# Kernel optimization log

Measured on AMD Instinct MI355X. Metric: run time of the kernel, lower is better.

## Reference

```python
import jax, jax.numpy as jnp
import numpy as np

EPS32 = np.float32(np.finfo(np.float32).eps)
N, D_IN = 8192, 256
LAYERS = [256, 128, 64]


def setup_inputs() -> dict:
    key = jax.random.key(0)
    ks = jax.random.split(key, 16)
    inp = {
        "feat_matrix": jax.random.normal(ks[0], (N, D_IN), dtype=jnp.float32),
        "adj_matrix": jnp.zeros((1,), jnp.float32),
        "get_item_index": jnp.zeros((1,), jnp.int64),
        "set_index": jnp.zeros((1,), jnp.int64),
        "val_index": jnp.zeros((1,), jnp.int64),
        "mask_matrix": jnp.zeros((1,), jnp.float32),
    }
    # Linear params for each (gl, gnn) pair, kaiming-ish scale 1/sqrt(fan_in)
    ki = 1
    for li in range(len(LAYERS) - 1):
        fi, fo = LAYERS[li], LAYERS[li + 1]
        s = 1.0 / np.sqrt(fi)
        inp[f"Wgl{li}"] = jax.random.uniform(ks[ki], (fi, fo), jnp.float32, -s, s); ki += 1
        inp[f"bgl{li}"] = jax.random.uniform(ks[ki], (fo,), jnp.float32, -s, s); ki += 1
        inp[f"Wgnn{li}"] = jax.random.uniform(ks[ki], (fi, fo), jnp.float32, -s, s); ki += 1
        inp[f"bgnn{li}"] = jax.random.uniform(ks[ki], (fo,), jnp.float32, -s, s); ki += 1
    inp["temp"] = jnp.float32(0.1)
    inp["theta"] = jnp.float32(0.1)
    return inp


def _cdgm_forward(x, params, temp, theta):
    n_layers = len(params)
    for k, (Wgl, bgl, Wgnn, bgnn) in enumerate(params):
        gl = jax.nn.relu(x @ Wgl + bgl)                      # [N, F]
        # pairwise squared distances without materializing [N, N, F]
        sq = jnp.sum(gl * gl, axis=-1)                       # [N]
        diff = jnp.maximum(sq[:, None] + sq[None, :] - 2.0 * (gl @ gl.T), 0.0)  # [N, N]
        mask = (diff != 0.0).astype(diff.dtype)
        dist = -jnp.sqrt(diff + EPS32) * mask
        adj = jax.nn.sigmoid((1.0 + temp) * dist + (5.0 + theta))  # [N, N]
        deg = jnp.sum(adj, axis=-1)                          # [N]; diag-inverse == rowwise divide
        x = (adj @ (x @ Wgnn + bgnn)) / deg[:, None]
        if k != n_layers - 1:
            x = jax.nn.relu(x)
    return jax.nn.softmax(x, axis=-1)


def reference(feat_matrix, adj_matrix, get_item_index, set_index, val_index, mask_matrix,
              Wgl0, bgl0, Wgnn0, bgnn0, Wgl1, bgl1, Wgnn1, bgnn1, temp, theta):
    params = [(Wgl0, bgl0, Wgnn0, bgnn0), (Wgl1, bgl1, Wgnn1, bgnn1)]
    return _cdgm_forward(feat_matrix, params, temp, theta)
```

## Files before the change

### kernel.cpp

```cpp
#include <hip/hip_runtime.h>
#include <hip/hip_bf16.h>

#define NROWS 8192

typedef __bf16 bf16x8 __attribute__((ext_vector_type(8)));
typedef float f32x4 __attribute__((ext_vector_type(4)));
typedef unsigned short ushort_t;
typedef unsigned int uint_t;

__device__ __forceinline__ ushort_t f2bf(float f) {
  uint_t u = __builtin_bit_cast(uint_t, f);
  u += 0x7fffu + ((u >> 16) & 1u);
  return (ushort_t)(u >> 16);
}
__device__ __forceinline__ float bf2f(ushort_t h) {
  uint_t u = ((uint_t)h) << 16;
  return __builtin_bit_cast(float, u);
}
__device__ __forceinline__ void load_lds16(const ushort_t* g, ushort_t* l) {
  __builtin_amdgcn_global_load_lds(
      (const __attribute__((address_space(1))) unsigned int*)g,
      (__attribute__((address_space(3))) unsigned int*)l, 16, 0, 0);
}
__device__ __forceinline__ void load_lds4(const float* g, float* l) {
  __builtin_amdgcn_global_load_lds(
      (const __attribute__((address_space(1))) unsigned int*)g,
      (__attribute__((address_space(3))) unsigned int*)l, 4, 0, 0);
}

template<int DIN, int F>
__global__ __launch_bounds__(256) void prep_w_kernel(
    const float* __restrict__ W1, const float* __restrict__ W2,
    ushort_t* __restrict__ Wf)
{
  constexpr int NCT = (2 * F) / 16;
  int idx = blockIdx.x * 256 + threadIdx.x;
  int e = idx & 7, lane = (idx >> 3) & 63;
  int ct = (idx >> 9) % NCT, kk = (idx >> 9) / NCT;
  int g = lane >> 4, q = lane & 15;
  int k = 32 * kk + 8 * g + e, c = 16 * ct + q;
  float v = (c < F) ? W1[(size_t)k * F + c] : W2[(size_t)k * F + (c - F)];
  Wf[idx] = f2bf(v);
}

template<int DIN, int F, bool RED>
__global__ __launch_bounds__(256) void lin_kernel(
    const float* __restrict__ x, const ushort_t* __restrict__ Wf,
    const float* __restrict__ b1, const float* __restrict__ b2,
    ushort_t* __restrict__ glf, float* __restrict__ sq, ushort_t* __restrict__ hf)
{
  constexpr int Fp   = F + 16;
  constexpr int NT   = Fp / 16;
  constexpr int KK   = F / 32;
  constexpr int KKD  = DIN / 32;
  constexpr int NCT  = (2 * F) / 16;
  constexpr int NCTW = NCT / 4;
  __shared__ float    xs[16][DIN];
  __shared__ float    hs[16][F];
  __shared__ ushort_t gls[16][F];
  __shared__ float    sqs[16];
  __shared__ float    degs[16];
  const int t  = threadIdx.x;
  const int m  = blockIdx.x;
  const int r0 = m * 16;
  const int w = t >> 6, lane = t & 63, g = lane >> 4, q = lane & 15;

  if (RED) {
    constexpr size_t STR = (size_t)NROWS * 144;
    if (t < 16) {
      float d = 0.f;
#pragma unroll
      for (int js = 0; js < 8; ++js)
        d += x[js * STR + (size_t)(r0 + t) * 144 + 128];
      degs[t] = d;
    }
    __syncthreads();
    for (int i = t; i < 16 * DIN; i += 256) {
      int r = i / DIN, c = i % DIN;
      float s = 0.f;
#pragma unroll
      for (int js = 0; js < 8; ++js)
        s += x[js * STR + (size_t)(r0 + r) * 144 + c];
      xs[r][c] = fmaxf(s, 0.f) / degs[r];
    }
  } else {
    for (int i = t; i < 16 * DIN; i += 256)
      xs[i / DIN][i % DIN] = x[(size_t)(r0 + i / DIN) * DIN + (i % DIN)];
  }
  if (t < 16) sqs[t] = 0.f;
  __syncthreads();

  bf16x8 aF[KKD];
#pragma unroll
  for (int kk = 0; kk < KKD; ++kk) {
    const float* src = &xs[q][32 * kk + 8 * g];
    __align__(16) ushort_t tmp[8];
#pragma unroll
    for (int e = 0; e < 8; ++e) tmp[e] = f2bf(src[e]);
    aF[kk] = *(const bf16x8*)tmp;
  }
  f32x4 acc[NCTW];
#pragma unroll
  for (int tl = 0; tl < NCTW; ++tl) {
    int c = 16 * (NCTW * w + tl) + q;
    float bv = (c < F) ? b1[c] : b2[c - F];
    acc[tl] = (f32x4){bv, bv, bv, bv};
  }
#pragma unroll
  for (int kk = 0; kk < KKD; ++kk)
#pragma unroll
    for (int tl = 0; tl < NCTW; ++tl) {
      bf16x8 bW = *(const bf16x8*)(Wf +
          ((size_t)(kk * NCT) + (NCTW * w + tl)) * 512 + lane * 8);
      acc[tl] = __builtin_amdgcn_mfma_f32_16x16x32_bf16(aF[kk], bW, acc[tl], 0, 0, 0);
    }
#pragma unroll
  for (int tl = 0; tl < NCTW; ++tl)
#pragma unroll
    for (int r = 0; r < 4; ++r) {
      int row = 4 * g + r, c = 16 * (NCTW * w + tl) + q;
      float v = acc[tl][r];
      if (c < F) {
        float gv = fmaxf(v, 0.f);
        ushort_t gb = f2bf(gv);
        gls[row][c] = gb;
        float gf = bf2f(gb);
        atomicAdd(&sqs[row], gf * gf);
      } else {
        hs[row][c - F] = v;
      }
    }
  __syncthreads();
  if (t < 16) sq[r0 + t] = sqs[t];

  {
    constexpr int CH = KK * 64;
    if (t < CH) {
      int kk = t >> 6, li = t & 63;
      int row = li & 15, c0 = 32 * kk + 8 * (li >> 4);
      uint4 v = *(const uint4*)&gls[row][c0];
      *(uint4*)(glf + ((size_t)(m * KK + kk) * 64 + li) * 8) = v;
    }
  }
  {
    const int jc  = m >> 2;
    const int P   = (m >> 1) & 1;
    const int glo = (m & 1) * 2;
    for (int idx = t; idx < NT * 32; idx += 256) {
      int t2 = idx >> 5, li = idx & 31;
      int gg = li >> 4, qq = li & 15;
      int feat = 16 * t2 + qq;
      ushort_t tmp[8];
#pragma unroll
      for (int e = 0; e < 8; ++e) {
        if (feat < F)        tmp[e] = f2bf(hs[8 * gg + e][feat]);
        else if (feat == F)  tmp[e] = (ushort_t)0x3F80;
        else                 tmp[e] = 0;
      }
      int ln = (glo + gg) * 16 + qq;
      uint4* dst = (uint4*)(hf + ((size_t)((jc * 2 + P) * NT + t2) * 64 + ln) * 8);
      *dst = *(const uint4*)tmp;
    }
  }
}

template<int F>
__global__ __launch_bounds__(256) void fused_kernel(
    const ushort_t* __restrict__ glf, const float* __restrict__ sq,
    const ushort_t* __restrict__ hf,
    const float* __restrict__ temp_p, const float* __restrict__ theta_p,
    float* __restrict__ partial)
{
  constexpr int Fp   = F + 16;
  constexpr int NT   = Fp / 16;
  constexpr int KK   = F / 32;
  constexpr int JS   = 8;
  constexpr int JCH  = NROWS / JS;
  constexpr int NIT  = JCH / 32;
  constexpr int NCHB = 2 * KK;
  constexpr int NHF  = NT - 1;
  constexpr int NCH  = NCHB + NHF;
  constexpr float EPS = 1.1920929e-07f;
  constexpr float LOG2E = 1.4426950408889634f;
  __shared__ __align__(16) ushort_t stage[NCH * 512 + 128];
  __shared__ __align__(16) ushort_t adjlds[128 * 32];

  const int w = threadIdx.x >> 6, lane = threadIdx.x & 63;
  const int g = lane >> 4, q = lane & 15;
  const int n  = blockIdx.x + (int)gridDim.x * blockIdx.y;
  const int bx = n >> 3, by = n & 7;
  const int irow  = bx * 128 + 32 * w;
  const int jbase = by * JCH;
  const float c1 = 1.0f + *temp_p;
  const float c0 = 5.0f + *theta_p;
  const float k1 = c1 * LOG2E;
  const float k0 = -c0 * LOG2E;

  bf16x8 aF[2][KK];
#pragma unroll
  for (int s = 0; s < 2; ++s)
#pragma unroll
    for (int kk = 0; kk < KK; ++kk)
      aF[s][kk] = *(const bf16x8*)(glf +
          ((size_t)(((irow >> 4) + s) * KK + kk) * 64 + lane) * 8);
  float sqi[2][4];
#pragma unroll
  for (int s = 0; s < 2; ++s)
#pragma unroll
    for (int r = 0; r < 4; ++r) sqi[s][r] = sq[irow + 16 * s + 4 * g + r] + EPS;

  bf16x8 onesF;
  {
    __align__(16) ushort_t tmp[8];
    ushort_t v = (q == 0) ? (ushort_t)0x3F80 : (ushort_t)0;
#pragma unroll
    for (int e = 0; e < 8; ++e) tmp[e] = v;
    onesF = *(const bf16x8*)tmp;
  }

  ushort_t* wp[8];
#pragma unroll
  for (int tt = 0; tt < 2; ++tt)
#pragma unroll
    for (int r = 0; r < 4; ++r) {
      int row = 32 * w + 4 * g + r;
      int colb = 32 * tt + 2 * q;
      wp[tt * 4 + r] = (ushort_t*)((char*)adjlds
                        + row * 64 + (colb ^ (((row >> 2) & 3) << 4)));
    }
  const ushort_t* rp;
  {
    int row = 32 * w + q;
    rp = (const ushort_t*)((char*)adjlds
          + row * 64 + ((16 * g) ^ (((row >> 2) & 3) << 4)));
  }
  const float* sql = (const float*)(stage + NCH * 512) + q;

  f32x4 acc[2][NT];
#pragma unroll
  for (int s = 0; s < 2; ++s)
#pragma unroll
    for (int i = 0; i < NT; ++i) acc[s][i] = (f32x4){0.f, 0.f, 0.f, 0.f};

#pragma unroll 1
  for (int k = 0; k < NIT; ++k) {
    const int j0 = jbase + k * 32;
    __syncthreads();
    {
      const ushort_t* glB = glf + (size_t)(j0 >> 4) * KK * 512;
      const ushort_t* glH = hf  + (size_t)(j0 >> 5) * NT * 512;
#pragma unroll
      for (int ch = w; ch < NCH; ch += 4) {
        const ushort_t* src = (ch < NCHB) ? (glB + (size_t)ch * 512)
                                          : (glH + (size_t)(ch - NCHB) * 512);
        load_lds16(src + lane * 8, stage + ch * 512);
      }
      if (w == 3 && lane < 32)
        load_lds4(sq + j0 + lane, (float*)(stage + NCH * 512) + lane);
    }
    __syncthreads();

    f32x4 sA[2][2];
    float sqj[2];
#pragma unroll
    for (int tt = 0; tt < 2; ++tt) {
      sqj[tt] = sql[16 * tt];
      f32x4 c0a = (f32x4){0.f, 0.f, 0.f, 0.f};
      f32x4 c1a = (f32x4){0.f, 0.f, 0.f, 0.f};
#pragma unroll
      for (int kk = 0; kk < KK; ++kk) {
        bf16x8 b = *(const bf16x8*)(stage + (tt * KK + kk) * 512 + lane * 8);
        c0a = __builtin_amdgcn_mfma_f32_16x16x32_bf16(aF[0][kk], b, c0a, 0, 0, 0);
        c1a = __builtin_amdgcn_mfma_f32_16x16x32_bf16(aF[1][kk], b, c1a, 0, 0, 0);
      }
      sA[0][tt] = c0a;
      sA[1][tt] = c1a;
    }
#pragma unroll
    for (int s = 0; s < 2; ++s)
#pragma unroll
      for (int tt = 0; tt < 2; ++tt)
#pragma unroll
        for (int r = 0; r < 4; ++r) {
          float t1 = sqi[s][r] + sqj[tt];
          float d  = fmaxf(fmaf(-2.f, sA[s][tt][r], t1), EPS);
          float e  = __builtin_amdgcn_exp2f(
                       fmaf(k1, __builtin_amdgcn_sqrtf(d), k0));
          float adjv = __builtin_amdgcn_rcpf(1.f + e);
          uint_t u = __builtin_bit_cast(uint_t, adjv) + 0x8000u;
          *(wp[tt * 4 + r] + s * 512) = (ushort_t)(u >> 16);
        }
    asm volatile("s_waitcnt lgkmcnt(0)" ::: "memory");
    {
      bf16x8 aP0 = *(const bf16x8*)(rp);
      bf16x8 aP1 = *(const bf16x8*)(rp + 512);
#pragma unroll
      for (int t2 = 0; t2 < NT; ++t2) {
        bf16x8 hF = (t2 == NT - 1)
            ? onesF
            : *(const bf16x8*)(stage + (NCHB + t2) * 512 + lane * 8);
        acc[0][t2] = __builtin_amdgcn_mfma_f32_16x16x32_bf16(aP0, hF, acc[0][t2], 0, 0, 0);
        acc[1][t2] = __builtin_amdgcn_mfma_f32_16x16x32_bf16(aP1, hF, acc[1][t2], 0, 0, 0);
      }
    }
  }

  float* op = partial + ((size_t)by * NROWS + irow) * Fp;
#pragma unroll
  for (int s = 0; s < 2; ++s)
#pragma unroll
    for (int t2 = 0; t2 < NT; ++t2)
#pragma unroll
      for (int r = 0; r < 4; ++r)
        op[(size_t)(16 * s + 4 * g + r) * Fp + 16 * t2 + q] = acc[s][t2][r];
}

__global__ __launch_bounds__(256) void reduce_softmax_kernel(
    const float* __restrict__ partial, float* __restrict__ out)
{
  int t = threadIdx.x;
  int r = blockIdx.x * 4 + (t >> 6), c = t & 63;
  size_t base = (size_t)r * 80;
  size_t stride = (size_t)NROWS * 80;
  float v = 0.f, d = 0.f;
#pragma unroll
  for (int js = 0; js < 8; ++js) {
    v += partial[js * stride + base + c];
    d += partial[js * stride + base + 64];
  }
  v /= d;
  float m = v;
  for (int o = 32; o > 0; o >>= 1) m = fmaxf(m, __shfl_xor(m, o, 64));
  float e = __expf(v - m);
  float s = e;
  for (int o = 32; o > 0; o >>= 1) s += __shfl_xor(s, o, 64);
  out[(size_t)r * 64 + c] = e / s;
}

extern "C" void kernel_launch(void* const* d_in, const int* in_sizes, int n_in,
                              void* d_out, int out_size, void* d_ws, size_t ws_size,
                              hipStream_t stream) {
  const float* feat  = (const float*)d_in[0];
  const float* Wgl0  = (const float*)d_in[6];
  const float* bgl0  = (const float*)d_in[7];
  const float* Wgnn0 = (const float*)d_in[8];
  const float* bgnn0 = (const float*)d_in[9];
  const float* Wgl1  = (const float*)d_in[10];
  const float* bgl1  = (const float*)d_in[11];
  const float* Wgnn1 = (const float*)d_in[12];
  const float* bgnn1 = (const float*)d_in[13];
  const float* temp  = (const float*)d_in[14];
  const float* theta = (const float*)d_in[15];
  float* out = (float*)d_out;

  char* ws = (char*)d_ws;
  size_t off = 0;
  auto alloc = [&](size_t bytes) {
    char* p = ws + off;
    off = (off + bytes + 255) & ~(size_t)255;
    return p;
  };
  float*    par0 = (float*)alloc(8ull * NROWS * 144 * 4);
  float*    par1 = par0;
  ushort_t* glf0 = (ushort_t*)alloc((8192ull / 16) * 4 * 64 * 8 * 2);
  ushort_t* glf1 = (ushort_t*)alloc((8192ull / 16) * 2 * 64 * 8 * 2);
  ushort_t* hf0  = (ushort_t*)alloc((8192ull / 64) * 2 * 9 * 64 * 8 * 2);
  ushort_t* hf1  = (ushort_t*)alloc((8192ull / 64) * 2 * 5 * 64 * 8 * 2);
  float*    sq0  = (float*)alloc(8192ull * 4);
  float*    sq1  = (float*)alloc(8192ull * 4);
  ushort_t* Wf0  = (ushort_t*)alloc(8ull * 16 * 512 * 2);
  ushort_t* Wf1  = (ushort_t*)alloc(4ull * 8 * 512 * 2);

  prep_w_kernel<256, 128><<<256, 256, 0, stream>>>(Wgl0, Wgnn0, Wf0);
  prep_w_kernel<128, 64><<<64, 256, 0, stream>>>(Wgl1, Wgnn1, Wf1);

  lin_kernel<256, 128, false><<<512, 256, 0, stream>>>(feat, Wf0, bgl0, bgnn0, glf0, sq0, hf0);
  fused_kernel<128><<<dim3(64, 8), 256, 0, stream>>>(glf0, sq0, hf0, temp, theta, par0);

  lin_kernel<128, 64, true><<<512, 256, 0, stream>>>(par0, Wf1, bgl1, bgnn1, glf1, sq1, hf1);
  fused_kernel<64><<<dim3(64, 8), 256, 0, stream>>>(glf1, sq1, hf1, temp, theta, par1);
  reduce_softmax_kernel<<<2048, 256, 0, stream>>>(par1, out);
}
```

Before: 142.6 us.

## Switch fused distance/aggregation kernel to 32x32x16 MFMA with in-register adjacency

The fused kernel now computes the pairwise Gram tile with 32x32x16 bf16 MFMA instead of 16x16x32. It converts the sigmoid adjacency values into the A-operand layout with packed bf16 conversion and permlane32 swaps, so the adjacency tile no longer goes through LDS. Its aim is to drop the LDS write/wait/read round trip and cut the MFMA issue count. The glf/hf staging layouts in lin_kernel and the partial-output stride (now padded to 32-column multiples) change to match, which adds some extra partial traffic and reduction work downstream.

```diff
diff --git a/kernel.cpp b/kernel.cpp
--- a/kernel.cpp
+++ b/kernel.cpp
@@ -5,6 +5,9 @@
 
 typedef __bf16 bf16x8 __attribute__((ext_vector_type(8)));
 typedef float f32x4 __attribute__((ext_vector_type(4)));
+typedef float f32x16 __attribute__((ext_vector_type(16)));
+typedef unsigned int u32x2 __attribute__((ext_vector_type(2)));
+typedef unsigned int u32x4 __attribute__((ext_vector_type(4)));
 typedef unsigned short ushort_t;
 typedef unsigned int uint_t;
 
@@ -16,6 +19,11 @@
 __device__ __forceinline__ float bf2f(ushort_t h) {
   uint_t u = ((uint_t)h) << 16;
   return __builtin_bit_cast(float, u);
+}
+__device__ __forceinline__ uint_t cvtpk(float lo, float hi) {
+  uint_t r;
+  asm("v_cvt_pk_bf16_f32 %0, %1, %2" : "=v"(r) : "v"(lo), "v"(hi));
+  return r;
 }
 __device__ __forceinline__ void load_lds16(const ushort_t* g, ushort_t* l) {
   __builtin_amdgcn_global_load_lds(
@@ -47,14 +55,12 @@
 __global__ __launch_bounds__(256) void lin_kernel(
     const float* __restrict__ x, const ushort_t* __restrict__ Wf,
     const float* __restrict__ b1, const float* __restrict__ b2,
-    ushort_t* __restrict__ glf, float* __restrict__ sq, ushort_t* __restrict__ hf)
+    ushort_t* __restrict__ glf32, float* __restrict__ sq, ushort_t* __restrict__ hf32)
 {
-  constexpr int Fp   = F + 16;
-  constexpr int NT   = Fp / 16;
-  constexpr int KK   = F / 32;
   constexpr int KKD  = DIN / 32;
   constexpr int NCT  = (2 * F) / 16;
   constexpr int NCTW = NCT / 4;
+  constexpr int FT   = F / 32;
   __shared__ float    xs[16][DIN];
   __shared__ float    hs[16][F];
   __shared__ ushort_t gls[16][F];
@@ -66,12 +72,12 @@
   const int w = t >> 6, lane = t & 63, g = lane >> 4, q = lane & 15;
 
   if (RED) {
-    constexpr size_t STR = (size_t)NROWS * 144;
+    constexpr size_t STR = (size_t)NROWS * 160;
     if (t < 16) {
       float d = 0.f;
 #pragma unroll
       for (int js = 0; js < 8; ++js)
-        d += x[js * STR + (size_t)(r0 + t) * 144 + 128];
+        d += x[js * STR + (size_t)(r0 + t) * 160 + 128];
       degs[t] = d;
     }
     __syncthreads();
@@ -80,7 +86,7 @@
       float s = 0.f;
 #pragma unroll
       for (int js = 0; js < 8; ++js)
-        s += x[js * STR + (size_t)(r0 + r) * 144 + c];
+        s += x[js * STR + (size_t)(r0 + r) * 160 + c];
       xs[r][c] = fmaxf(s, 0.f) / degs[r];
     }
   } else {
@@ -133,60 +139,43 @@
   __syncthreads();
   if (t < 16) sq[r0 + t] = sqs[t];
 
-  {
-    constexpr int CH = KK * 64;
-    if (t < CH) {
-      int kk = t >> 6, li = t & 63;
-      int row = li & 15, c0 = 32 * kk + 8 * (li >> 4);
-      uint4 v = *(const uint4*)&gls[row][c0];
-      *(uint4*)(glf + ((size_t)(m * KK + kk) * 64 + li) * 8) = v;
-    }
-  }
-  {
-    const int jc  = m >> 2;
-    const int P   = (m >> 1) & 1;
-    const int glo = (m & 1) * 2;
-    for (int idx = t; idx < NT * 32; idx += 256) {
-      int t2 = idx >> 5, li = idx & 31;
-      int gg = li >> 4, qq = li & 15;
-      int feat = 16 * t2 + qq;
-      ushort_t tmp[8];
-#pragma unroll
-      for (int e = 0; e < 8; ++e) {
-        if (feat < F)        tmp[e] = f2bf(hs[8 * gg + e][feat]);
-        else if (feat == F)  tmp[e] = (ushort_t)0x3F80;
-        else                 tmp[e] = 0;
-      }
-      int ln = (glo + gg) * 16 + qq;
-      uint4* dst = (uint4*)(hf + ((size_t)((jc * 2 + P) * NT + t2) * 64 + ln) * 8);
-      *dst = *(const uint4*)tmp;
-    }
+  if (t < 32 * (F / 16)) {
+    int ch = t >> 5, li = t & 31;
+    int lane2 = 32 * (li >> 4) + 16 * (m & 1) + (li & 15);
+    const uint4* src = (const uint4*)&gls[li & 15][16 * ch + 8 * (li >> 4)];
+    *(uint4*)(glf32 + ((size_t)(m >> 1) * (F / 16) + ch) * 512 + lane2 * 8) = *src;
+  }
+  if (t < FT * 64) {
+    int ft = t >> 6, l2 = t & 63;
+    __align__(16) ushort_t tmp[8];
+#pragma unroll
+    for (int e = 0; e < 8; ++e)
+      tmp[e] = f2bf(hs[8 * (l2 >> 5) + e][32 * ft + (l2 & 31)]);
+    *(uint4*)(hf32 + ((size_t)m * FT + ft) * 512 + l2 * 8) = *(const uint4*)tmp;
   }
 }
 
 template<int F>
 __global__ __launch_bounds__(256) void fused_kernel(
-    const ushort_t* __restrict__ glf, const float* __restrict__ sq,
-    const ushort_t* __restrict__ hf,
+    const ushort_t* __restrict__ glf32, const float* __restrict__ sq,
+    const ushort_t* __restrict__ hf32,
     const float* __restrict__ temp_p, const float* __restrict__ theta_p,
     float* __restrict__ partial)
 {
-  constexpr int Fp   = F + 16;
-  constexpr int NT   = Fp / 16;
-  constexpr int KK   = F / 32;
+  constexpr int FT   = F / 32;
+  constexpr int FpO  = 32 * (FT + 1);
+  constexpr int KKW  = F / 16;
   constexpr int JS   = 8;
   constexpr int JCH  = NROWS / JS;
   constexpr int NIT  = JCH / 32;
-  constexpr int NCHB = 2 * KK;
-  constexpr int NHF  = NT - 1;
-  constexpr int NCH  = NCHB + NHF;
+  constexpr int NCHB = KKW;
+  constexpr int NCH  = NCHB + 2 * FT;
   constexpr float EPS = 1.1920929e-07f;
   constexpr float LOG2E = 1.4426950408889634f;
   __shared__ __align__(16) ushort_t stage[NCH * 512 + 128];
-  __shared__ __align__(16) ushort_t adjlds[128 * 32];
 
   const int w = threadIdx.x >> 6, lane = threadIdx.x & 63;
-  const int g = lane >> 4, q = lane & 15;
+  const int hi = lane >> 5, col = lane & 31;
   const int n  = blockIdx.x + (int)gridDim.x * blockIdx.y;
   const int bx = n >> 3, by = n & 7;
   const int irow  = bx * 128 + 32 * w;
@@ -196,59 +185,37 @@
   const float k1 = c1 * LOG2E;
   const float k0 = -c0 * LOG2E;
 
-  bf16x8 aF[2][KK];
-#pragma unroll
-  for (int s = 0; s < 2; ++s)
-#pragma unroll
-    for (int kk = 0; kk < KK; ++kk)
-      aF[s][kk] = *(const bf16x8*)(glf +
-          ((size_t)(((irow >> 4) + s) * KK + kk) * 64 + lane) * 8);
-  float sqi[2][4];
-#pragma unroll
-  for (int s = 0; s < 2; ++s)
-#pragma unroll
-    for (int r = 0; r < 4; ++r) sqi[s][r] = sq[irow + 16 * s + 4 * g + r] + EPS;
+  bf16x8 iF[KKW];
+#pragma unroll
+  for (int kk = 0; kk < KKW; ++kk)
+    iF[kk] = *(const bf16x8*)(glf32 +
+        ((size_t)(irow >> 5) * KKW + kk) * 512 + lane * 8);
+  const float sqi = sq[irow + col] + EPS;
 
   bf16x8 onesF;
   {
     __align__(16) ushort_t tmp[8];
-    ushort_t v = (q == 0) ? (ushort_t)0x3F80 : (ushort_t)0;
+    ushort_t v = (col == 0) ? (ushort_t)0x3F80 : (ushort_t)0;
 #pragma unroll
     for (int e = 0; e < 8; ++e) tmp[e] = v;
     onesF = *(const bf16x8*)tmp;
   }
 
-  ushort_t* wp[8];
-#pragma unroll
-  for (int tt = 0; tt < 2; ++tt)
-#pragma unroll
-    for (int r = 0; r < 4; ++r) {
-      int row = 32 * w + 4 * g + r;
-      int colb = 32 * tt + 2 * q;
-      wp[tt * 4 + r] = (ushort_t*)((char*)adjlds
-                        + row * 64 + (colb ^ (((row >> 2) & 3) << 4)));
-    }
-  const ushort_t* rp;
-  {
-    int row = 32 * w + q;
-    rp = (const ushort_t*)((char*)adjlds
-          + row * 64 + ((16 * g) ^ (((row >> 2) & 3) << 4)));
-  }
-  const float* sql = (const float*)(stage + NCH * 512) + q;
-
-  f32x4 acc[2][NT];
-#pragma unroll
-  for (int s = 0; s < 2; ++s)
-#pragma unroll
-    for (int i = 0; i < NT; ++i) acc[s][i] = (f32x4){0.f, 0.f, 0.f, 0.f};
+  f32x16 acc[FT + 1];
+#pragma unroll
+  for (int ft = 0; ft <= FT; ++ft)
+#pragma unroll
+    for (int r = 0; r < 16; ++r) acc[ft][r] = 0.f;
+
+  const float* sqlane = (const float*)(stage + NCH * 512) + 4 * hi;
 
 #pragma unroll 1
   for (int k = 0; k < NIT; ++k) {
     const int j0 = jbase + k * 32;
     __syncthreads();
     {
-      const ushort_t* glB = glf + (size_t)(j0 >> 4) * KK * 512;
-      const ushort_t* glH = hf  + (size_t)(j0 >> 5) * NT * 512;
+      const ushort_t* glB = glf32 + (size_t)(j0 >> 5) * KKW * 512;
+      const ushort_t* glH = hf32  + (size_t)(j0 >> 4) * FT * 512;
 #pragma unroll
       for (int ch = w; ch < NCH; ch += 4) {
         const ushort_t* src = (ch < NCHB) ? (glB + (size_t)ch * 512)
@@ -260,59 +227,58 @@
     }
     __syncthreads();
 
-    f32x4 sA[2][2];
-    float sqj[2];
-#pragma unroll
-    for (int tt = 0; tt < 2; ++tt) {
-      sqj[tt] = sql[16 * tt];
-      f32x4 c0a = (f32x4){0.f, 0.f, 0.f, 0.f};
-      f32x4 c1a = (f32x4){0.f, 0.f, 0.f, 0.f};
-#pragma unroll
-      for (int kk = 0; kk < KK; ++kk) {
-        bf16x8 b = *(const bf16x8*)(stage + (tt * KK + kk) * 512 + lane * 8);
-        c0a = __builtin_amdgcn_mfma_f32_16x16x32_bf16(aF[0][kk], b, c0a, 0, 0, 0);
-        c1a = __builtin_amdgcn_mfma_f32_16x16x32_bf16(aF[1][kk], b, c1a, 0, 0, 0);
+    f32x16 sacc;
+#pragma unroll
+    for (int r = 0; r < 16; ++r) sacc[r] = 0.f;
+#pragma unroll
+    for (int kk = 0; kk < KKW; ++kk) {
+      bf16x8 jf = *(const bf16x8*)(stage + kk * 512 + lane * 8);
+      sacc = __builtin_amdgcn_mfma_f32_32x32x16_bf16(jf, iF[kk], sacc, 0, 0, 0);
+    }
+    f32x4 sqjv[4];
+#pragma unroll
+    for (int G = 0; G < 4; ++G) sqjv[G] = *(const f32x4*)(sqlane + 8 * G);
+    float adjv[16];
+#pragma unroll
+    for (int r = 0; r < 16; ++r) {
+      float t1 = sqi + sqjv[r >> 2][r & 3];
+      float d  = fmaxf(fmaf(-2.f, sacc[r], t1), EPS);
+      float e  = __builtin_amdgcn_exp2f(fmaf(k1, __builtin_amdgcn_sqrtf(d), k0));
+      adjv[r] = __builtin_amdgcn_rcpf(1.f + e);
+    }
+    uint_t P0 = cvtpk(adjv[0],  adjv[1]),  P1 = cvtpk(adjv[2],  adjv[3]);
+    uint_t P2 = cvtpk(adjv[4],  adjv[5]),  P3 = cvtpk(adjv[6],  adjv[7]);
+    uint_t P4 = cvtpk(adjv[8],  adjv[9]),  P5 = cvtpk(adjv[10], adjv[11]);
+    uint_t P6 = cvtpk(adjv[12], adjv[13]), P7 = cvtpk(adjv[14], adjv[15]);
+    u32x2 sA0 = __builtin_amdgcn_permlane32_swap(P2, P0, false, false);
+    u32x2 sA1 = __builtin_amdgcn_permlane32_swap(P3, P1, false, false);
+    u32x2 sB0 = __builtin_amdgcn_permlane32_swap(P6, P4, false, false);
+    u32x2 sB1 = __builtin_amdgcn_permlane32_swap(P7, P5, false, false);
+    u32x4 dw1 = {sA0[1], sA1[1], sA0[0], sA1[0]};
+    u32x4 dw2 = {sB0[1], sB1[1], sB0[0], sB1[0]};
+    bf16x8 PA1 = __builtin_bit_cast(bf16x8, dw1);
+    bf16x8 PA2 = __builtin_bit_cast(bf16x8, dw2);
+#pragma unroll
+    for (int o = 0; o < 2; ++o) {
+      bf16x8 PA = o ? PA2 : PA1;
+#pragma unroll
+      for (int ft = 0; ft <= FT; ++ft) {
+        bf16x8 hfr = (ft == FT)
+            ? onesF
+            : *(const bf16x8*)(stage + (NCHB + o * FT + ft) * 512 + lane * 8);
+        acc[ft] = __builtin_amdgcn_mfma_f32_32x32x16_bf16(PA, hfr, acc[ft], 0, 0, 0);
       }
-      sA[0][tt] = c0a;
-      sA[1][tt] = c1a;
-    }
-#pragma unroll
-    for (int s = 0; s < 2; ++s)
-#pragma unroll
-      for (int tt = 0; tt < 2; ++tt)
-#pragma unroll
-        for (int r = 0; r < 4; ++r) {
-          float t1 = sqi[s][r] + sqj[tt];
-          float d  = fmaxf(fmaf(-2.f, sA[s][tt][r], t1), EPS);
-          float e  = __builtin_amdgcn_exp2f(
-                       fmaf(k1, __builtin_amdgcn_sqrtf(d), k0));
-          float adjv = __builtin_amdgcn_rcpf(1.f + e);
-          uint_t u = __builtin_bit_cast(uint_t, adjv) + 0x8000u;
-          *(wp[tt * 4 + r] + s * 512) = (ushort_t)(u >> 16);
-        }
-    asm volatile("s_waitcnt lgkmcnt(0)" ::: "memory");
-    {
-      bf16x8 aP0 = *(const bf16x8*)(rp);
-      bf16x8 aP1 = *(const bf16x8*)(rp + 512);
-#pragma unroll
-      for (int t2 = 0; t2 < NT; ++t2) {
-        bf16x8 hF = (t2 == NT - 1)
-            ? onesF
-            : *(const bf16x8*)(stage + (NCHB + t2) * 512 + lane * 8);
-        acc[0][t2] = __builtin_amdgcn_mfma_f32_16x16x32_bf16(aP0, hF, acc[0][t2], 0, 0, 0);
-        acc[1][t2] = __builtin_amdgcn_mfma_f32_16x16x32_bf16(aP1, hF, acc[1][t2], 0, 0, 0);
-      }
-    }
-  }
-
-  float* op = partial + ((size_t)by * NROWS + irow) * Fp;
-#pragma unroll
-  for (int s = 0; s < 2; ++s)
-#pragma unroll
-    for (int t2 = 0; t2 < NT; ++t2)
-#pragma unroll
-      for (int r = 0; r < 4; ++r)
-        op[(size_t)(16 * s + 4 * g + r) * Fp + 16 * t2 + q] = acc[s][t2][r];
+    }
+  }
+
+  float* op = partial + ((size_t)by * NROWS + irow) * FpO + col;
+#pragma unroll
+  for (int ft = 0; ft <= FT; ++ft)
+#pragma unroll
+    for (int r = 0; r < 16; ++r) {
+      int row = (r & 3) + 8 * (r >> 2) + 4 * hi;
+      op[(size_t)row * FpO + 32 * ft] = acc[ft][r];
+    }
 }
 
 __global__ __launch_bounds__(256) void reduce_softmax_kernel(
@@ -320,8 +286,8 @@
 {
   int t = threadIdx.x;
   int r = blockIdx.x * 4 + (t >> 6), c = t & 63;
-  size_t base = (size_t)r * 80;
-  size_t stride = (size_t)NROWS * 80;
+  size_t base = (size_t)r * 96;
+  size_t stride = (size_t)NROWS * 96;
   float v = 0.f, d = 0.f;
 #pragma unroll
   for (int js = 0; js < 8; ++js) {
@@ -360,12 +326,12 @@
     off = (off + bytes + 255) & ~(size_t)255;
     return p;
   };
-  float*    par0 = (float*)alloc(8ull * NROWS * 144 * 4);
+  float*    par0 = (float*)alloc(8ull * NROWS * 160 * 4);
   float*    par1 = par0;
-  ushort_t* glf0 = (ushort_t*)alloc((8192ull / 16) * 4 * 64 * 8 * 2);
-  ushort_t* glf1 = (ushort_t*)alloc((8192ull / 16) * 2 * 64 * 8 * 2);
-  ushort_t* hf0  = (ushort_t*)alloc((8192ull / 64) * 2 * 9 * 64 * 8 * 2);
-  ushort_t* hf1  = (ushort_t*)alloc((8192ull / 64) * 2 * 5 * 64 * 8 * 2);
+  ushort_t* glf0 = (ushort_t*)alloc((8192ull / 32) * 8 * 512 * 2);
+  ushort_t* glf1 = (ushort_t*)alloc((8192ull / 32) * 4 * 512 * 2);
+  ushort_t* hf0  = (ushort_t*)alloc((8192ull / 16) * 4 * 512 * 2);
+  ushort_t* hf1  = (ushort_t*)alloc((8192ull / 16) * 2 * 512 * 2);
   float*    sq0  = (float*)alloc(8192ull * 4);
   float*    sq1  = (float*)alloc(8192ull * 4);
   ushort_t* Wf0  = (ushort_t*)alloc(8ull * 16 * 512 * 2);
```

New measurement: 146.7 us. +2.9%, slower.
